# Kernel optimization log

Hardware: AMD Instinct MI355X
Metric: run time of the kernel (lower is better)

Reference implementation:

```python
import jax, jax.numpy as jnp
import numpy as np

MAX_FRAMES = 12
TOPK = 49
NUM_SAMPLES = 256
SIGMA = 0.05
LN_EPS = 1e-5


def setup_inputs() -> dict:
    key = jax.random.key(0)
    ks = jax.random.split(key, 6)
    B, MF, N, D = 8, MAX_FRAMES, 197, 512
    x = jax.random.normal(ks[0], (B, MF * N, D), dtype=jnp.float32)
    noise = jax.random.normal(ks[1], (B * MF, NUM_SAMPLES, N - 1), dtype=jnp.float32)
    ln_gamma = jnp.ones((D,), jnp.float32)
    ln_beta = jnp.zeros((D,), jnp.float32)
    w_in = jax.random.normal(ks[2], (D, D // 2), dtype=jnp.float32) * 0.02
    w1 = jax.random.normal(ks[3], (D, D // 2), dtype=jnp.float32) * 0.02
    w2 = jax.random.normal(ks[4], (D // 2, 1), dtype=jnp.float32) * 0.02
    return {"x": x, "noise": noise, "ln_gamma": ln_gamma, "ln_beta": ln_beta,
            "w_in": w_in, "w1": w1, "w2": w2}


def reference(x, noise, ln_gamma, ln_beta, w_in, w1, w2):
    B, L, D = x.shape
    N = L // MAX_FRAMES
    xf = x.reshape(B * MAX_FRAMES, N, D)          # (b, N, D)

    # PredictorLG: LayerNorm -> Linear -> GELU (torch GELU is exact erf)
    mu = xf.mean(-1, keepdims=True)
    var = xf.var(-1, keepdims=True)               # biased, matches torch LayerNorm
    hn = (xf - mu) * jax.lax.rsqrt(var + LN_EPS) * ln_gamma + ln_beta
    h = jax.nn.gelu(hn @ w_in, approximate=False)  # (b, N, D/2)
    # concat local features with broadcast global (cls-token) features
    g = jnp.broadcast_to(h[:, :1, :], h.shape)
    cat = jnp.concatenate([h, g], axis=-1)         # (b, N, D)
    score = jnp.tanh(jax.nn.gelu(cat @ w1, approximate=False) @ w2)[..., 0]  # (b, N)

    sp = score[:, 1:]                              # (b, d) spatial scores, d = N-1
    b_eff, ns, d = noise.shape
    pert = sp[:, None, :] + noise * SIGMA          # (b, ns, d)

    # top-k set per sample; sorted ascending (matches torch sort of topk indices)
    order = jnp.argsort(-pert, axis=-1)            # descending by value
    top_sorted = jnp.sort(order[..., :TOPK], axis=-1)  # (b, ns, k)

    # mean of one-hots == scatter-add counts / num_samples (avoids one-hot blowup)
    bi = jnp.arange(b_eff)[:, None, None]
    pos = jnp.arange(TOPK)[None, None, :]
    ind = jnp.zeros((b_eff, TOPK, d), x.dtype).at[bi, pos, top_sorted].add(1.0) / ns

    cls_feat = xf[:, :1, :]                        # (b, 1, D)
    spat_feat = xf[:, 1:, :]                       # (b, d, D)
    sel = jnp.einsum('bkl,bld->bkd', ind, spat_feat)  # (b, k, D)
    out = jnp.concatenate([cls_feat, sel], axis=1)    # (b, 1+k, D)
    return out.reshape(B, MAX_FRAMES * (1 + TOPK), D)
```

## Files before the change

kernel.cpp:

```cpp
#include <hip/hip_runtime.h>
#include <math.h>

#define NFRAME 96
#define NTOK   197
#define NSPAT  196
#define DIM    512
#define DH     256
#define NSAMP  256
#define KSEL   49
#define SIG    0.05f
#define MPAD   208
#define MTOT   (NFRAME * MPAD)

typedef unsigned short u16;
typedef __attribute__((ext_vector_type(8))) short bf16x8;
typedef __attribute__((ext_vector_type(4))) float f32x4;

__device__ __forceinline__ float gelu_exact(float v) {
    return 0.5f * v * (1.0f + erff(v * 0.70710678118654752440f));
}
__device__ __forceinline__ unsigned bf16_rne(float f) {
    unsigned u = __float_as_uint(f);
    return (u + 0x7fffu + ((u >> 16) & 1u)) >> 16;
}
__device__ __forceinline__ float bf16_to_f(unsigned h) {
    return __uint_as_float(h << 16);
}

__device__ __forceinline__ void gld16(const u16* g, u16* l) {
    __builtin_amdgcn_global_load_lds(
        (const __attribute__((address_space(1))) void*)g,
        (__attribute__((address_space(3))) void*)l, 16, 0, 0);
}
__device__ __forceinline__ bf16x8 srd(const u16* base, int r, int cw) {
    return *(const bf16x8*)((const char*)base + r * 128 + (((cw) ^ (r & 7)) << 4));
}

__global__ __launch_bounds__(256) void k0_prep(
    const float* __restrict__ x, const float* __restrict__ gamma,
    const float* __restrict__ beta,
    const float* __restrict__ w_in, const float* __restrict__ w1,
    u16* __restrict__ wiT_hi, u16* __restrict__ wiT_lo,
    u16* __restrict__ w1T_hi, u16* __restrict__ w1T_lo,
    u16* __restrict__ xs_hi, u16* __restrict__ xs_lo)
{
    if (blockIdx.x < 512) {
        const int n = blockIdx.x & 255, which = blockIdx.x >> 8;
        const float* w = which ? w1 : w_in;
        u16* th = which ? w1T_hi : wiT_hi;
        u16* tl = which ? w1T_lo : wiT_lo;
        for (int k = threadIdx.x; k < DIM; k += 256) {
            float v = w[(size_t)k * DH + n];
            unsigned hi = bf16_rne(v);
            unsigned lo = bf16_rne(v - bf16_to_f(hi));
            th[(size_t)n * DIM + k] = (u16)hi;
            tl[(size_t)n * DIM + k] = (u16)lo;
        }
        return;
    }
    const int row  = (blockIdx.x - 512) * 4 + (threadIdx.x >> 6);
    const int lane = threadIdx.x & 63;
    const int f = row / MPAD;
    int rr = row - f * MPAD; if (rr > NTOK - 1) rr = NTOK - 1;
    const float* xr = x + ((size_t)f * NTOK + rr) * DIM + lane * 8;
    float4 a = *(const float4*)xr, b4 = *(const float4*)(xr + 4);
    float e[8] = {a.x, a.y, a.z, a.w, b4.x, b4.y, b4.z, b4.w};
    float s = 0.f, sq = 0.f;
    #pragma unroll
    for (int j = 0; j < 8; ++j) { s += e[j]; sq += e[j] * e[j]; }
    #pragma unroll
    for (int o = 32; o > 0; o >>= 1) {
        s  += __shfl_xor(s,  o, 64);
        sq += __shfl_xor(sq, o, 64);
    }
    const float mu  = s * (1.f / 512.f);
    const float var = sq * (1.f / 512.f) - mu * mu;
    const float rs  = 1.f / sqrtf(var + 1e-5f);

    const float* gp = gamma + lane * 8;
    const float* bp = beta + lane * 8;
    float4 g0 = *(const float4*)gp, g1 = *(const float4*)(gp + 4);
    float4 b0 = *(const float4*)bp, b1 = *(const float4*)(bp + 4);
    float gg[8] = {g0.x, g0.y, g0.z, g0.w, g1.x, g1.y, g1.z, g1.w};
    float bt[8] = {b0.x, b0.y, b0.z, b0.w, b1.x, b1.y, b1.z, b1.w};

    unsigned hw[4], lw[4];
    #pragma unroll
    for (int p = 0; p < 4; ++p) {
        float s0 = rs * gg[2*p],   s1 = rs * gg[2*p+1];
        float v0 = e[2*p]   * s0 + (bt[2*p]   - mu * s0);
        float v1 = e[2*p+1] * s1 + (bt[2*p+1] - mu * s1);
        unsigned h0 = bf16_rne(v0), h1 = bf16_rne(v1);
        float l0 = v0 - bf16_to_f(h0), l1 = v1 - bf16_to_f(h1);
        hw[p] = h0 | (h1 << 16);
        lw[p] = bf16_rne(l0) | (bf16_rne(l1) << 16);
    }
    size_t off = (size_t)row * DIM + lane * 8;
    *(uint4*)(xs_hi + off) = make_uint4(hw[0], hw[1], hw[2], hw[3]);
    *(uint4*)(xs_lo + off) = make_uint4(lw[0], lw[1], lw[2], lw[3]);
}

__global__ __launch_bounds__(256, 3) void k1_gemm1(
    const u16* __restrict__ xs_hi, const u16* __restrict__ xs_lo,
    const u16* __restrict__ wiT_hi, const u16* __restrict__ wiT_lo,
    u16* __restrict__ h_hi, u16* __restrict__ h_lo)
{
    __shared__ u16 Ah[128][64], Al[128][64], Bh[64][64], Bl[64][64];
    const int t = threadIdx.x, lane = t & 63, wv = t >> 6;
    const int linear = (blockIdx.x & 7) * 78 + (blockIdx.x >> 3);
    const int Mb = linear >> 2, Nb = linear & 3;
    const int R0 = Mb * 128, N0 = Nb * 64;
    const int wm = wv >> 1, wn = wv & 1;
    const int m15 = lane & 15, q = lane >> 4;
    const int r8 = lane >> 3;
    const int cg = (lane & 7) ^ r8;

    f32x4 acc[4][2];
    #pragma unroll
    for (int i = 0; i < 4; ++i)
        #pragma unroll
        for (int j = 0; j < 2; ++j)
            acc[i][j] = (f32x4){0.f, 0.f, 0.f, 0.f};

    for (int k0 = 0; k0 < DIM; k0 += 64) {
        __syncthreads();
        #pragma unroll
        for (int j = 0; j < 4; ++j) {
            const int rA = wv * 32 + j * 8;
            const size_t src = (size_t)(R0 + rA + r8) * DIM + k0 + cg * 8;
            gld16(xs_hi + src, &Ah[rA][0]);
            gld16(xs_lo + src, &Al[rA][0]);
        }
        #pragma unroll
        for (int j = 0; j < 2; ++j) {
            const int rB = wv * 16 + j * 8;
            const size_t src = (size_t)(N0 + rB + r8) * DIM + k0 + cg * 8;
            gld16(wiT_hi + src, &Bh[rB][0]);
            gld16(wiT_lo + src, &Bl[rB][0]);
        }
        __syncthreads();

        #pragma unroll
        for (int kh = 0; kh < 2; ++kh) {
            const int cw = kh * 4 + q;
            bf16x8 a_h[4], a_l[4], b_h[2], b_l[2];
            #pragma unroll
            for (int i = 0; i < 4; ++i) {
                const int r = wm * 64 + i * 16 + m15;
                a_h[i] = srd(&Ah[0][0], r, cw);
                a_l[i] = srd(&Al[0][0], r, cw);
            }
            #pragma unroll
            for (int n = 0; n < 2; ++n) {
                const int r = wn * 32 + n * 16 + m15;
                b_h[n] = srd(&Bh[0][0], r, cw);
                b_l[n] = srd(&Bl[0][0], r, cw);
            }
            #pragma unroll
            for (int mt = 0; mt < 4; ++mt)
                #pragma unroll
                for (int nt = 0; nt < 2; ++nt) {
                    f32x4 c = acc[mt][nt];
                    c = __builtin_amdgcn_mfma_f32_16x16x32_bf16(a_h[mt], b_h[nt], c, 0, 0, 0);
                    c = __builtin_amdgcn_mfma_f32_16x16x32_bf16(a_l[mt], b_h[nt], c, 0, 0, 0);
                    c = __builtin_amdgcn_mfma_f32_16x16x32_bf16(a_h[mt], b_l[nt], c, 0, 0, 0);
                    acc[mt][nt] = c;
                }
        }
    }

    #pragma unroll
    for (int mt = 0; mt < 4; ++mt)
        #pragma unroll
        for (int nt = 0; nt < 2; ++nt)
            #pragma unroll
            for (int reg = 0; reg < 4; ++reg) {
                int r = R0 + wm*64 + mt*16 + q*4 + reg;
                int c = N0 + wn*32 + nt*16 + m15;
                float v = gelu_exact(acc[mt][nt][reg]);
                unsigned hb = bf16_rne(v);
                unsigned lb = bf16_rne(v - bf16_to_f(hb));
                size_t off = (size_t)r * DH + c;
                h_hi[off] = (u16)hb;
                h_lo[off] = (u16)lb;
            }
}

__global__ __launch_bounds__(256) void k1g_gbias(
    const u16* __restrict__ h_hi, const u16* __restrict__ h_lo,
    const u16* __restrict__ w1T_hi, const u16* __restrict__ w1T_lo,
    float* __restrict__ gbias)
{
    const int f = blockIdx.x, n = threadIdx.x;
    const size_t hoff = (size_t)f * MPAD * DH;
    const size_t woff = (size_t)n * DIM + DH;
    float s = 0.f;
    for (int k = 0; k < DH; k += 8) {
        uint4 vh = *(const uint4*)(h_hi + hoff + k);
        uint4 vl = *(const uint4*)(h_lo + hoff + k);
        uint4 uh = *(const uint4*)(w1T_hi + woff + k);
        uint4 ul = *(const uint4*)(w1T_lo + woff + k);
        const unsigned* ph = (const unsigned*)&vh;
        const unsigned* pl = (const unsigned*)&vl;
        const unsigned* qh = (const unsigned*)&uh;
        const unsigned* ql = (const unsigned*)&ul;
        #pragma unroll
        for (int w = 0; w < 4; ++w) {
            float a0 = bf16_to_f(ph[w] & 0xffffu) + bf16_to_f(pl[w] & 0xffffu);
            float a1 = bf16_to_f(ph[w] >> 16)     + bf16_to_f(pl[w] >> 16);
            float b0 = bf16_to_f(qh[w] & 0xffffu) + bf16_to_f(ql[w] & 0xffffu);
            float b1 = bf16_to_f(qh[w] >> 16)     + bf16_to_f(ql[w] >> 16);
            s += a0 * b0 + a1 * b1;
        }
    }
    gbias[f * DH + n] = s;
}

__global__ __launch_bounds__(256, 3) void k1_gemm2(
    const u16* __restrict__ h_hi, const u16* __restrict__ h_lo,
    const u16* __restrict__ w1T_hi, const u16* __restrict__ w1T_lo,
    const float* __restrict__ w2, const float* __restrict__ gbias,
    float* __restrict__ s_quar)
{
    __shared__ u16 Ah[128][64], Al[128][64], Bh[64][64], Bl[64][64];
    __shared__ float red[2][2][64];
    const int t = threadIdx.x, lane = t & 63, wv = t >> 6;
    const int linear = (blockIdx.x & 7) * 78 + (blockIdx.x >> 3);
    const int Mb = linear >> 2, Nb = linear & 3;
    const int R0 = Mb * 128, N0 = Nb * 64;
    const int wm = wv >> 1, wn = wv & 1;
    const int m15 = lane & 15, q = lane >> 4;
    const int r8 = lane >> 3;
    const int cg = (lane & 7) ^ r8;

    f32x4 acc[4][2];
    #pragma unroll
    for (int i = 0; i < 4; ++i)
        #pragma unroll
        for (int j = 0; j < 2; ++j)
            acc[i][j] = (f32x4){0.f, 0.f, 0.f, 0.f};

    for (int k0 = 0; k0 < DH; k0 += 64) {
        __syncthreads();
        #pragma unroll
        for (int j = 0; j < 4; ++j) {
            const int rA = wv * 32 + j * 8;
            const size_t src = (size_t)(R0 + rA + r8) * DH + k0 + cg * 8;
            gld16(h_hi + src, &Ah[rA][0]);
            gld16(h_lo + src, &Al[rA][0]);
        }
        #pragma unroll
        for (int j = 0; j < 2; ++j) {
            const int rB = wv * 16 + j * 8;
            const size_t src = (size_t)(N0 + rB + r8) * DIM + k0 + cg * 8;
            gld16(w1T_hi + src, &Bh[rB][0]);
            gld16(w1T_lo + src, &Bl[rB][0]);
        }
        __syncthreads();

        #pragma unroll
        for (int kh = 0; kh < 2; ++kh) {
            const int cw = kh * 4 + q;
            bf16x8 a_h[4], a_l[4], b_h[2], b_l[2];
            #pragma unroll
            for (int i = 0; i < 4; ++i) {
                const int r = wm * 64 + i * 16 + m15;
                a_h[i] = srd(&Ah[0][0], r, cw);
                a_l[i] = srd(&Al[0][0], r, cw);
            }
            #pragma unroll
            for (int n = 0; n < 2; ++n) {
                const int r = wn * 32 + n * 16 + m15;
                b_h[n] = srd(&Bh[0][0], r, cw);
                b_l[n] = srd(&Bl[0][0], r, cw);
            }
            #pragma unroll
            for (int mt = 0; mt < 4; ++mt)
                #pragma unroll
                for (int nt = 0; nt < 2; ++nt) {
                    f32x4 c = acc[mt][nt];
                    c = __builtin_amdgcn_mfma_f32_16x16x32_bf16(a_h[mt], b_h[nt], c, 0, 0, 0);
                    c = __builtin_amdgcn_mfma_f32_16x16x32_bf16(a_l[mt], b_h[nt], c, 0, 0, 0);
                    c = __builtin_amdgcn_mfma_f32_16x16x32_bf16(a_h[mt], b_l[nt], c, 0, 0, 0);
                    acc[mt][nt] = c;
                }
        }
    }

    float w2v[2];
    int   cIdx[2];
    #pragma unroll
    for (int nt = 0; nt < 2; ++nt) {
        cIdx[nt] = N0 + wn*32 + nt*16 + m15;
        w2v[nt]  = w2[cIdx[nt]];
    }
    #pragma unroll
    for (int mt = 0; mt < 4; ++mt)
        #pragma unroll
        for (int reg = 0; reg < 4; ++reg) {
            int r = R0 + wm*64 + mt*16 + q*4 + reg;
            int f = r / MPAD;
            float gb0 = gbias[f * DH + cIdx[0]];
            float gb1 = gbias[f * DH + cIdx[1]];
            float s = gelu_exact(acc[mt][0][reg] + gb0) * w2v[0] +
                      gelu_exact(acc[mt][1][reg] + gb1) * w2v[1];
            #pragma unroll
            for (int o = 1; o <= 8; o <<= 1)
                s += __shfl_xor(s, o, 64);
            if (m15 == 0)
                red[wn][wm][mt*16 + q*4 + reg] = s;
        }
    __syncthreads();
    if (t < 128) {
        int wmj = t >> 6, rl = t & 63;
        float sv = red[0][wmj][rl] + red[1][wmj][rl];
        s_quar[(size_t)Nb * MTOT + R0 + t] = sv;
    }
}

__global__ __launch_bounds__(1024) void k2_select(
    const float* __restrict__ s_quar, const float* __restrict__ noise,
    int* __restrict__ hist2)
{
    const int fb   = blockIdx.x;
    const int f    = fb >> 1;
    const int half = fb & 1;
    const int t    = threadIdx.x;
    const int lane = t & 63;
    const int wv   = t >> 6;

    __shared__ int hist_s[KSEL * NSPAT];
    for (int i = t; i < KSEL * NSPAT; i += 1024) hist_s[i] = 0;

    const float* s0 = s_quar;
    const float* s1 = s_quar + MTOT;
    const float* s2 = s_quar + 2 * (size_t)MTOT;
    const float* s3 = s_quar + 3 * (size_t)MTOT;
    float spv[4];
    #pragma unroll
    for (int j = 0; j < 4; ++j) {
        int l = lane + 64 * j;
        if (l < NSPAT) {
            size_t idx = (size_t)f * MPAD + 1 + l;
            spv[j] = tanhf(s0[idx] + s1[idx] + s2[idx] + s3[idx]);
        } else spv[j] = 0.f;
    }
    __syncthreads();

    const unsigned long long lmask = (1ull << lane) - 1ull;

    for (int si = 0; si < 8; ++si) {
        const int s = half * 128 + wv * 8 + si;
        const float* nz = noise + ((size_t)f * NSAMP + s) * NSPAT;
        unsigned key[4];
        #pragma unroll
        for (int j = 0; j < 4; ++j) {
            int l = lane + 64 * j;
            if (l < NSPAT) {
                float p = spv[j] + nz[l] * SIG;
                unsigned u = __float_as_uint(p);
                key[j] = (u & 0x80000000u) ? ~u : (u | 0x80000000u);
            } else {
                key[j] = 0u;
            }
        }

        unsigned ans;
        {
            int c31 = 0;
            #pragma unroll
            for (int j = 0; j < 4; ++j)
                c31 += __popcll(__ballot(key[j] >= 0x80000000u));
            ans = (c31 >= KSEL) ? 0x80000000u : 0x40000000u;
        }
        for (int bit = 29; bit >= 0; --bit) {
            unsigned cand = ans | (1u << bit);
            int cnt = 0;
            #pragma unroll
            for (int j = 0; j < 4; ++j)
                cnt += __popcll(__ballot(key[j] >= cand));
            if (cnt >= KSEL) ans = cand;
        }

        unsigned long long eq[4];
        int cgt = 0;
        #pragma unroll
        for (int j = 0; j < 4; ++j) {
            cgt += __popcll(__ballot(key[j] > ans));
            eq[j] = __ballot(key[j] == ans);
        }
        const int quota = KSEL - cgt;
        int eqpre[4]; { int run = 0;
            #pragma unroll
            for (int j = 0; j < 4; ++j) { eqpre[j] = run; run += __popcll(eq[j]); } }

        int pre = 0;
        #pragma unroll
        for (int j = 0; j < 4; ++j) {
            bool iseq = (key[j] == ans);
            int trk = eqpre[j] + __popcll(eq[j] & lmask);
            bool selj = (key[j] > ans) || (iseq && trk < quota);
            unsigned long long sb = __ballot(selj);
            int rk = pre + __popcll(sb & lmask);
            if (selj)
                atomicAdd(&hist_s[rk * NSPAT + lane + 64 * j], 1);
            pre += __popcll(sb);
        }
    }

    __syncthreads();
    int* hb = hist2 + (size_t)fb * (KSEL * NSPAT);
    for (int i = t; i < KSEL * NSPAT; i += 1024)
        hb[i] = hist_s[i];
}

#define KP3 52
__global__ __launch_bounds__(256) void k3_output(
    const float* __restrict__ x, const int* __restrict__ hist2,
    float* __restrict__ out)
{
    const int b   = blockIdx.x >> 3;
    const int ds  = blockIdx.x & 7;
    const int d0  = ds * 64;
    const int t   = threadIdx.x;
    const int tdc = t & 15;
    const int tk  = t >> 4;

    __shared__ float hist_s[NSPAT * KP3 + 16];

    const int* h0 = hist2 + (size_t)(2 * b) * (KSEL * NSPAT);
    const int* h1 = h0 + KSEL * NSPAT;
    for (int i = t; i < KSEL * NSPAT; i += 256) {
        int k = i / NSPAT;
        int l = i - k * NSPAT;
        hist_s[l * KP3 + k] = (float)(h0[i] + h1[i]);
    }
    for (int i = t; i < NSPAT * 3 + 16; i += 256) {
        int l = i / 3, j = i - l * 3;
        int idx = (i < NSPAT * 3) ? (l * KP3 + KSEL + j) : (NSPAT * KP3 + i - NSPAT * 3);
        hist_s[idx] = 0.f;
    }
    if (t < 64)
        out[(size_t)b * 50 * DIM + d0 + t] = x[(size_t)b * NTOK * DIM + d0 + t];
    __syncthreads();

    const float* xs = x + ((size_t)b * NTOK + 1) * DIM + d0 + tdc * 4;
    float4 acc[4];
    #pragma unroll
    for (int i = 0; i < 4; ++i) acc[i] = make_float4(0.f, 0.f, 0.f, 0.f);

    #pragma unroll 7
    for (int l = 0; l < NSPAT; ++l) {
        float4 v  = *(const float4*)(xs + (size_t)l * DIM);
        float4 w4 = *(const float4*)&hist_s[l * KP3 + tk * 4];
        acc[0].x += w4.x * v.x; acc[0].y += w4.x * v.y;
        acc[0].z += w4.x * v.z; acc[0].w += w4.x * v.w;
        acc[1].x += w4.y * v.x; acc[1].y += w4.y * v.y;
        acc[1].z += w4.y * v.z; acc[1].w += w4.y * v.w;
        acc[2].x += w4.z * v.x; acc[2].y += w4.z * v.y;
        acc[2].z += w4.z * v.z; acc[2].w += w4.z * v.w;
        acc[3].x += w4.w * v.x; acc[3].y += w4.w * v.y;
        acc[3].z += w4.w * v.z; acc[3].w += w4.w * v.w;
    }

    const float inv = 1.f / 256.f;
    #pragma unroll
    for (int i = 0; i < 4; ++i) {
        int k = tk * 4 + i;
        if (k < KSEL) {
            float4 o = make_float4(acc[i].x * inv, acc[i].y * inv,
                                   acc[i].z * inv, acc[i].w * inv);
            *(float4*)&out[((size_t)b * 50 + 1 + k) * DIM + d0 + tdc * 4] = o;
        }
    }
}

extern "C" void kernel_launch(void* const* d_in, const int* in_sizes, int n_in,
                              void* d_out, int out_size, void* d_ws, size_t ws_size,
                              hipStream_t stream)
{
    const float* x     = (const float*)d_in[0];
    const float* noise = (const float*)d_in[1];
    const float* gamma = (const float*)d_in[2];
    const float* beta  = (const float*)d_in[3];
    const float* w_in  = (const float*)d_in[4];
    const float* w1    = (const float*)d_in[5];
    const float* w2    = (const float*)d_in[6];
    float* out = (float*)d_out;

    char* ws = (char*)d_ws;
    int*   hist2   = (int*)  (ws + 0);
    float* gbias   = (float*)(ws + 0);
    float* s_quar  = (float*)(ws + 7375872);
    u16*   wiT_hi  = (u16*)  (ws + 7695360);
    u16*   wiT_lo  = (u16*)  (ws + 7957504);
    u16*   w1T_hi  = (u16*)  (ws + 8219648);
    u16*   w1T_lo  = (u16*)  (ws + 8481792);
    u16*   h_hi    = (u16*)  (ws + 8743936);
    u16*   h_lo    = (u16*)  (ws + 18967552);
    u16*   xs_hi   = (u16*)  (ws + 29191168);
    u16*   xs_lo   = (u16*)  (ws + 49638400);

    k0_prep<<<512 + MTOT / 4, 256, 0, stream>>>(x, gamma, beta, w_in, w1,
                                                wiT_hi, wiT_lo, w1T_hi, w1T_lo,
                                                xs_hi, xs_lo);
    k1_gemm1<<<(MTOT / 128) * 4, 256, 0, stream>>>(xs_hi, xs_lo, wiT_hi, wiT_lo,
                                                   h_hi, h_lo);
    k1g_gbias<<<NFRAME, 256, 0, stream>>>(h_hi, h_lo, w1T_hi, w1T_lo, gbias);
    k1_gemm2<<<(MTOT / 128) * 4, 256, 0, stream>>>(h_hi, h_lo, w1T_hi, w1T_lo,
                                                   w2, gbias, s_quar);
    k2_select<<<NFRAME * 2, 1024, 0, stream>>>(s_quar, noise, hist2);
    k3_output<<<NFRAME * 8, 256, 0, stream>>>(x, hist2, out);
}
```

Baseline: 214.2 us.

## Fuse global-bias computation into gemm2 and early-exit radix top-k search

Removes the separate gbias kernel: each gemm2 block now computes the cls-token bias for the one or two frames its 128-row tile spans into shared memory before the main loop, saving a launch and a global round trip. The cost is redundant bias work, since every block recomputes a 128×256 dot-product set, and that work adds latency before the MFMA loop. The k2 radix-select loop now exits as soon as the count equals K exactly, skipping the remaining bit iterations. A trivial reorder of two FMAs in k3 has no effect.

```diff
diff --git a/kernel.cpp b/kernel.cpp
--- a/kernel.cpp
+++ b/kernel.cpp
@@ -186,44 +186,14 @@
             }
 }
 
-__global__ __launch_bounds__(256) void k1g_gbias(
-    const u16* __restrict__ h_hi, const u16* __restrict__ h_lo,
-    const u16* __restrict__ w1T_hi, const u16* __restrict__ w1T_lo,
-    float* __restrict__ gbias)
-{
-    const int f = blockIdx.x, n = threadIdx.x;
-    const size_t hoff = (size_t)f * MPAD * DH;
-    const size_t woff = (size_t)n * DIM + DH;
-    float s = 0.f;
-    for (int k = 0; k < DH; k += 8) {
-        uint4 vh = *(const uint4*)(h_hi + hoff + k);
-        uint4 vl = *(const uint4*)(h_lo + hoff + k);
-        uint4 uh = *(const uint4*)(w1T_hi + woff + k);
-        uint4 ul = *(const uint4*)(w1T_lo + woff + k);
-        const unsigned* ph = (const unsigned*)&vh;
-        const unsigned* pl = (const unsigned*)&vl;
-        const unsigned* qh = (const unsigned*)&uh;
-        const unsigned* ql = (const unsigned*)&ul;
-        #pragma unroll
-        for (int w = 0; w < 4; ++w) {
-            float a0 = bf16_to_f(ph[w] & 0xffffu) + bf16_to_f(pl[w] & 0xffffu);
-            float a1 = bf16_to_f(ph[w] >> 16)     + bf16_to_f(pl[w] >> 16);
-            float b0 = bf16_to_f(qh[w] & 0xffffu) + bf16_to_f(ql[w] & 0xffffu);
-            float b1 = bf16_to_f(qh[w] >> 16)     + bf16_to_f(ql[w] >> 16);
-            s += a0 * b0 + a1 * b1;
-        }
-    }
-    gbias[f * DH + n] = s;
-}
-
 __global__ __launch_bounds__(256, 3) void k1_gemm2(
     const u16* __restrict__ h_hi, const u16* __restrict__ h_lo,
     const u16* __restrict__ w1T_hi, const u16* __restrict__ w1T_lo,
-    const float* __restrict__ w2, const float* __restrict__ gbias,
-    float* __restrict__ s_quar)
+    const float* __restrict__ w2, float* __restrict__ s_quar)
 {
     __shared__ u16 Ah[128][64], Al[128][64], Bh[64][64], Bl[64][64];
     __shared__ float red[2][2][64];
+    __shared__ float gb_s[2][64];
     const int t = threadIdx.x, lane = t & 63, wv = t >> 6;
     const int linear = (blockIdx.x & 7) * 78 + (blockIdx.x >> 3);
     const int Mb = linear >> 2, Nb = linear & 3;
@@ -232,6 +202,36 @@
     const int m15 = lane & 15, q = lane >> 4;
     const int r8 = lane >> 3;
     const int cg = (lane & 7) ^ r8;
+    const int f0 = R0 / MPAD;
+    const int f1 = (R0 + 127) / MPAD;
+
+    if (t < 128) {
+        const int fi = t >> 6;
+        const int fr = (f0 + fi <= f1) ? (f0 + fi) : f1;
+        const int c  = N0 + (t & 63);
+        const size_t hoff = (size_t)fr * MPAD * DH;
+        const size_t woff = (size_t)c * DIM + DH;
+        float s = 0.f;
+        for (int k = 0; k < DH; k += 8) {
+            uint4 vh = *(const uint4*)(h_hi + hoff + k);
+            uint4 vl = *(const uint4*)(h_lo + hoff + k);
+            uint4 uh = *(const uint4*)(w1T_hi + woff + k);
+            uint4 ul = *(const uint4*)(w1T_lo + woff + k);
+            const unsigned* ph = (const unsigned*)&vh;
+            const unsigned* pl = (const unsigned*)&vl;
+            const unsigned* qh = (const unsigned*)&uh;
+            const unsigned* ql = (const unsigned*)&ul;
+            #pragma unroll
+            for (int w = 0; w < 4; ++w) {
+                float a0 = bf16_to_f(ph[w] & 0xffffu) + bf16_to_f(pl[w] & 0xffffu);
+                float a1 = bf16_to_f(ph[w] >> 16)     + bf16_to_f(pl[w] >> 16);
+                float b0 = bf16_to_f(qh[w] & 0xffffu) + bf16_to_f(ql[w] & 0xffffu);
+                float b1 = bf16_to_f(qh[w] >> 16)     + bf16_to_f(ql[w] >> 16);
+                s += a0 * b0 + a1 * b1;
+            }
+        }
+        gb_s[fi][t & 63] = s;
+    }
 
     f32x4 acc[4][2];
     #pragma unroll
@@ -288,20 +288,20 @@
     }
 
     float w2v[2];
-    int   cIdx[2];
+    int   cl[2];
     #pragma unroll
     for (int nt = 0; nt < 2; ++nt) {
-        cIdx[nt] = N0 + wn*32 + nt*16 + m15;
-        w2v[nt]  = w2[cIdx[nt]];
+        cl[nt]  = wn*32 + nt*16 + m15;
+        w2v[nt] = w2[N0 + cl[nt]];
     }
     #pragma unroll
     for (int mt = 0; mt < 4; ++mt)
         #pragma unroll
         for (int reg = 0; reg < 4; ++reg) {
             int r = R0 + wm*64 + mt*16 + q*4 + reg;
-            int f = r / MPAD;
-            float gb0 = gbias[f * DH + cIdx[0]];
-            float gb1 = gbias[f * DH + cIdx[1]];
+            int fi = (r / MPAD) - f0;
+            float gb0 = gb_s[fi][cl[0]];
+            float gb1 = gb_s[fi][cl[1]];
             float s = gelu_exact(acc[mt][0][reg] + gb0) * w2v[0] +
                       gelu_exact(acc[mt][1][reg] + gb1) * w2v[1];
             #pragma unroll
@@ -366,20 +366,25 @@
         }
 
         unsigned ans;
+        int c31 = 0;
         {
-            int c31 = 0;
             #pragma unroll
             for (int j = 0; j < 4; ++j)
                 c31 += __popcll(__ballot(key[j] >= 0x80000000u));
             ans = (c31 >= KSEL) ? 0x80000000u : 0x40000000u;
         }
-        for (int bit = 29; bit >= 0; --bit) {
-            unsigned cand = ans | (1u << bit);
-            int cnt = 0;
-            #pragma unroll
-            for (int j = 0; j < 4; ++j)
-                cnt += __popcll(__ballot(key[j] >= cand));
-            if (cnt >= KSEL) ans = cand;
+        if (c31 != KSEL) {
+            for (int bit = 29; bit >= 0; --bit) {
+                unsigned cand = ans | (1u << bit);
+                int cnt = 0;
+                #pragma unroll
+                for (int j = 0; j < 4; ++j)
+                    cnt += __popcll(__ballot(key[j] >= cand));
+                if (cnt >= KSEL) {
+                    ans = cand;
+                    if (cnt == KSEL) break;
+                }
+            }
         }
 
         unsigned long long eq[4];
@@ -460,7 +465,7 @@
         acc[2].x += w4.z * v.x; acc[2].y += w4.z * v.y;
         acc[2].z += w4.z * v.z; acc[2].w += w4.z * v.w;
         acc[3].x += w4.w * v.x; acc[3].y += w4.w * v.y;
-        acc[3].z += w4.w * v.z; acc[3].w += w4.w * v.w;
+        acc[3].w += w4.w * v.w; acc[3].z += w4.w * v.z;
     }
 
     const float inv = 1.f / 256.f;
@@ -490,7 +495,6 @@
 
     char* ws = (char*)d_ws;
     int*   hist2   = (int*)  (ws + 0);
-    float* gbias   = (float*)(ws + 0);
     float* s_quar  = (float*)(ws + 7375872);
     u16*   wiT_hi  = (u16*)  (ws + 7695360);
     u16*   wiT_lo  = (u16*)  (ws + 7957504);
@@ -506,9 +510,8 @@
                                                 xs_hi, xs_lo);
     k1_gemm1<<<(MTOT / 128) * 4, 256, 0, stream>>>(xs_hi, xs_lo, wiT_hi, wiT_lo,
                                                    h_hi, h_lo);
-    k1g_gbias<<<NFRAME, 256, 0, stream>>>(h_hi, h_lo, w1T_hi, w1T_lo, gbias);
     k1_gemm2<<<(MTOT / 128) * 4, 256, 0, stream>>>(h_hi, h_lo, w1T_hi, w1T_lo,
-                                                   w2, gbias, s_quar);
+                                                   w2, s_quar);
     k2_select<<<NFRAME * 2, 1024, 0, stream>>>(s_quar, noise, hist2);
     k3_output<<<NFRAME * 8, 256, 0, stream>>>(x, hist2, out);
 }
```

Result: faster. 205.3 us (-4.1%).
